# Performance work log

Measured on AMD Instinct MI355X. Metric: run time of the kernel, lower is better.

The kernel has to match this reference:

```python
import jax, jax.numpy as jnp
import numpy as np

EPS = 1e-12  # torch F.normalize eps


def _l1_normalize(x, axis):
    denom = jnp.maximum(jnp.sum(jnp.abs(x), axis=axis, keepdims=True), EPS)
    return x / denom


def setup_inputs() -> dict:
    key = jax.random.key(0)
    k1, k2, k3, k4, k5 = jax.random.split(key, 5)
    B, N, M, F_atom, F_bond, F_out = 16, 1024, 12, 128, 32, 128
    stdv = 1.0 / np.sqrt(F_out)
    atom = jax.random.normal(k1, (B, N, F_atom), dtype=jnp.float32)
    bond = jax.random.normal(k2, (B, N, M, F_bond), dtype=jnp.float32)
    adj_matrix = jax.random.randint(k3, (B, N, M), 0, N, dtype=jnp.int64)
    weight_atom_1 = jax.random.uniform(k4, (F_atom, F_out), dtype=jnp.float32, minval=-stdv, maxval=stdv)
    bias_atom_1 = jax.random.uniform(k5, (F_out,), dtype=jnp.float32, minval=-stdv, maxval=stdv)
    return {
        "atom": atom,
        "bond": bond,
        "adj_matrix": adj_matrix,
        "weight_atom_1": weight_atom_1,
        "bias_atom_1": bias_atom_1,
    }


def reference(atom, bond, adj_matrix, weight_atom_1, bias_atom_1):
    # atom: (B,N,F); bond: (B,N,M,Fb); adj_matrix: (B,N,M)
    # Per-batch neighbor gather: atom_neighbor[b,n,m] = atom[b, adj[b,n,m]]
    atom_neighbor = jax.vmap(lambda a, idx: a[idx])(atom, adj_matrix)  # (B,N,M,F)
    atom_neighbor = jnp.mean(atom_neighbor, axis=-2)  # (B,N,F)

    # Bond-norm chain
    bond_norm = jnp.sqrt(jnp.sum(bond * bond, axis=-1))       # (B,N,M) L2 norm
    bond_norm = bond_norm ** (-2.0)                            # inverse square
    bond_norm = _l1_normalize(bond_norm, axis=-1)              # over M
    bond_norm = jnp.prod(bond_norm, axis=2)                    # (B,N)
    bond_norm = _l1_normalize(bond_norm, axis=0)               # over B
    bond_norm = bond_norm ** (-1.0)
    bond_norm = _l1_normalize(bond_norm, axis=1)               # over N

    atom_update = (atom + atom_neighbor) * bond_norm[:, :, None]
    atom_update = jnp.matmul(atom_update, weight_atom_1) + bias_atom_1
    return jax.nn.relu(atom_update)
```

## Files before the change

kernel.cpp:

```cpp
#include <hip/hip_runtime.h>
#include <hip/hip_bf16.h>

#define EPS 1e-12f

typedef __bf16 bf16x8 __attribute__((ext_vector_type(8)));
typedef float  f32x4  __attribute__((ext_vector_type(4)));


__global__ __launch_bounds__(256) void k_bond(const float* __restrict__ bond,
                                              const float* __restrict__ W,
                                              float* __restrict__ p_out,
                                              __bf16* __restrict__ Wt) {
    const int t = threadIdx.x;
    if (blockIdx.x < 256) {
        const int gtid = blockIdx.x * 256 + t;
        const int row  = gtid >> 2;
        const int q    = gtid & 3;
        const float* base = bond + (size_t)row * 384 + q * 96;

        float x[3];
#pragma unroll
        for (int mm = 0; mm < 3; ++mm) {
            float s = 0.f;
#pragma unroll
            for (int j = 0; j < 8; ++j) {
                f32x4 v = *(const f32x4*)(base + mm * 32 + j * 4);
                s = fmaf(v.x, v.x, s);
                s = fmaf(v.y, v.y, s);
                s = fmaf(v.z, v.z, s);
                s = fmaf(v.w, v.w, s);
            }
            x[mm] = 1.0f / s;
        }
        float sum  = x[0] + x[1] + x[2];
        float prod = x[0] * x[1] * x[2];
        sum  += __shfl_xor(sum, 1);  prod *= __shfl_xor(prod, 1);
        sum  += __shfl_xor(sum, 2);  prod *= __shfl_xor(prod, 2);
        if (q == 0) {
            float d   = fmaxf(sum, EPS);
            float d2  = d * d;
            float d3  = d2 * d;
            float d6  = d3 * d3;
            float d12 = d6 * d6;
            p_out[row] = prod / d12;
        }
    } else {
        const int base = (blockIdx.x - 256) * 4096;
#pragma unroll
        for (int i = 0; i < 16; ++i) {
            int idx = base + t + 256 * i;
            int k = idx >> 7, j = idx & 127;
            Wt[j * 128 + k] = (__bf16)W[idx];
        }
    }
}

__global__ __launch_bounds__(256) void k_main(const float* __restrict__ atom,
                                              const int* __restrict__ adj,
                                              const float* __restrict__ p,
                                              const __bf16* __restrict__ Wt,
                                              const float* __restrict__ bias,
                                              float* __restrict__ out) {
    __shared__ __bf16 uA[32][136];
    __shared__ float  sScale[32];
    __shared__ int    sAdj[32 * 12];
    __shared__ float  red[4];

    const int t = threadIdx.x;
    const int rowbase = blockIdx.x * 32;
    const int b = rowbase >> 10;

    for (int idx = t; idx < 32 * 12; idx += 256) sAdj[idx] = adj[rowbase * 12 + idx];

    float S_part = 0.f;
#pragma unroll
    for (int i = 0; i < 4; ++i) {
        int n = t + 256 * i;
        float cs = 0.f;
#pragma unroll
        for (int bb = 0; bb < 16; ++bb) cs += p[bb * 1024 + n];
        S_part += fmaxf(cs, EPS) / p[b * 1024 + n];
    }
#pragma unroll
    for (int off = 32; off >= 1; off >>= 1) S_part += __shfl_xor(S_part, off);
    if ((t & 63) == 0) red[t >> 6] = S_part;
    __syncthreads();
    const float S = fmaxf(red[0] + red[1] + red[2] + red[3], EPS);
    if (t < 32) {
        int nl = (rowbase & 1023) + t;
        float cs = 0.f;
#pragma unroll
        for (int bb = 0; bb < 16; ++bb) cs += p[bb * 1024 + nl];
        sScale[t] = (fmaxf(cs, EPS) / p[rowbase + t]) / S;
    }
    __syncthreads();

    {
        const int j = t & 127;
        const int half = t >> 7;
        const float* atomB = atom + (size_t)b * (1024 * 128);
#pragma unroll 4
        for (int r = half; r < 32; r += 2) {
            float accn = 0.f;
#pragma unroll
            for (int m = 0; m < 12; ++m) {
                int idx = sAdj[r * 12 + m];
                accn += atomB[idx * 128 + j];
            }
            float u = (atom[(size_t)(rowbase + r) * 128 + j] + accn * (1.0f / 12.0f)) * sScale[r];
            uA[r][j] = (__bf16)u;
        }
    }
    __syncthreads();

    const int wave = t >> 6, lane = t & 63;
    const int r0 = (wave >> 1) * 16;
    const int c0 = (wave & 1) * 64;
    const int quad = lane >> 4, lrow = lane & 15;

    bf16x8 aF[4];
#pragma unroll
    for (int kc = 0; kc < 4; ++kc)
        aF[kc] = *(const bf16x8*)&uA[r0 + lrow][kc * 32 + quad * 8];

    f32x4 acc[4];
#pragma unroll
    for (int nt = 0; nt < 4; ++nt) acc[nt] = (f32x4){0.f, 0.f, 0.f, 0.f};

#pragma unroll
    for (int nt = 0; nt < 4; ++nt) {
        const int col = c0 + nt * 16 + lrow;
        const __bf16* wb = Wt + col * 128 + quad * 8;
#pragma unroll
        for (int kc = 0; kc < 4; ++kc) {
            bf16x8 bF = *(const bf16x8*)(wb + kc * 32);
            acc[nt] = __builtin_amdgcn_mfma_f32_16x16x32_bf16(aF[kc], bF, acc[nt], 0, 0, 0);
        }
    }

#pragma unroll
    for (int nt = 0; nt < 4; ++nt) {
        const int col = c0 + nt * 16 + lrow;
        const float bv = bias[col];
#pragma unroll
        for (int i = 0; i < 4; ++i) {
            const int r = r0 + quad * 4 + i;
            float v = fmaxf(acc[nt][i] + bv, 0.f);
            __builtin_nontemporal_store(v, &out[(size_t)(rowbase + r) * 128 + col]);
        }
    }
}

extern "C" void kernel_launch(void* const* d_in, const int* in_sizes, int n_in,
                              void* d_out, int out_size, void* d_ws, size_t ws_size,
                              hipStream_t stream) {
    const float* atom = (const float*)d_in[0];
    const float* bond = (const float*)d_in[1];
    const int*   adj  = (const int*)d_in[2];
    const float* W    = (const float*)d_in[3];
    const float* bias = (const float*)d_in[4];
    float* out = (float*)d_out;

    char* ws = (char*)d_ws;
    float*  p  = (float*)ws;
    __bf16* Wt = (__bf16*)(ws + 65536);

    hipLaunchKernelGGL(k_bond, dim3(260), dim3(256), 0, stream, bond, W, p, Wt);
    hipLaunchKernelGGL(k_main, dim3(512), dim3(256), 0, stream, atom, adj, p, Wt, bias, out);
}
```

Measured before the change: 104.5 us.

## Vectorize neighbor gather, move row scale after MFMA, overlap p loads

Measured after the change: 116.8 us. 11.8% more time.

```diff
diff --git a/kernel.cpp b/kernel.cpp
--- a/kernel.cpp
+++ b/kernel.cpp
@@ -4,6 +4,7 @@
 #define EPS 1e-12f
 
 typedef __bf16 bf16x8 __attribute__((ext_vector_type(8)));
+typedef __bf16 bf16x4 __attribute__((ext_vector_type(4)));
 typedef float  f32x4  __attribute__((ext_vector_type(4)));
 
 
@@ -24,7 +25,7 @@
             float s = 0.f;
 #pragma unroll
             for (int j = 0; j < 8; ++j) {
-                f32x4 v = *(const f32x4*)(base + mm * 32 + j * 4);
+                f32x4 v = __builtin_nontemporal_load((const f32x4*)(base + mm * 32 + j * 4));
                 s = fmaf(v.x, v.x, s);
                 s = fmaf(v.y, v.y, s);
                 s = fmaf(v.z, v.z, s);
@@ -38,11 +39,8 @@
         sum  += __shfl_xor(sum, 2);  prod *= __shfl_xor(prod, 2);
         if (q == 0) {
             float d   = fmaxf(sum, EPS);
-            float d2  = d * d;
-            float d3  = d2 * d;
-            float d6  = d3 * d3;
-            float d12 = d6 * d6;
-            p_out[row] = prod / d12;
+            float d2  = d * d, d3 = d2 * d, d6 = d3 * d3;
+            p_out[row] = prod / (d6 * d6);
         }
     } else {
         const int base = (blockIdx.x - 256) * 4096;
@@ -62,56 +60,66 @@
                                               const float* __restrict__ bias,
                                               float* __restrict__ out) {
     __shared__ __bf16 uA[32][136];
-    __shared__ float  sScale[32];
+    __shared__ float  sScale[32] __attribute__((aligned(16)));
     __shared__ int    sAdj[32 * 12];
     __shared__ float  red[4];
 
     const int t = threadIdx.x;
     const int rowbase = blockIdx.x * 32;
     const int b = rowbase >> 10;
+    const int nlo = rowbase & 1023;
+
+    const int n0 = t * 4;
+    f32x4 cs = {0.f, 0.f, 0.f, 0.f};
+    f32x4 pv[16];
+#pragma unroll
+    for (int bb = 0; bb < 16; ++bb) pv[bb] = *(const f32x4*)(p + bb * 1024 + n0);
 
     for (int idx = t; idx < 32 * 12; idx += 256) sAdj[idx] = adj[rowbase * 12 + idx];
+    __syncthreads();
 
-    float S_part = 0.f;
+    const int jc = (t & 31) * 4;
+    const int rg = t >> 5;
+    const float* atomB = atom + (size_t)b * (1024 * 128);
+    f32x4 own[4], accn[4];
 #pragma unroll
     for (int i = 0; i < 4; ++i) {
-        int n = t + 256 * i;
-        float cs = 0.f;
+        const int r = rg + i * 8;
+        f32x4 a = {0.f, 0.f, 0.f, 0.f};
 #pragma unroll
-        for (int bb = 0; bb < 16; ++bb) cs += p[bb * 1024 + n];
-        S_part += fmaxf(cs, EPS) / p[b * 1024 + n];
+        for (int m = 0; m < 12; ++m) {
+            int idx = sAdj[r * 12 + m];
+            a += *(const f32x4*)(atomB + (size_t)idx * 128 + jc);
+        }
+        accn[i] = a;
+        own[i]  = *(const f32x4*)(atomB + (size_t)(nlo + r) * 128 + jc);
     }
+
+#pragma unroll
+    for (int bb = 0; bb < 16; ++bb) cs += pv[bb];
+    f32x4 pb = pv[b];
+    f32x4 r4;
+    r4.x = fmaxf(cs.x, EPS) / pb.x;
+    r4.y = fmaxf(cs.y, EPS) / pb.y;
+    r4.z = fmaxf(cs.z, EPS) / pb.z;
+    r4.w = fmaxf(cs.w, EPS) / pb.w;
+    float S_part = r4.x + r4.y + r4.z + r4.w;
 #pragma unroll
     for (int off = 32; off >= 1; off >>= 1) S_part += __shfl_xor(S_part, off);
     if ((t & 63) == 0) red[t >> 6] = S_part;
-    __syncthreads();
-    const float S = fmaxf(red[0] + red[1] + red[2] + red[3], EPS);
-    if (t < 32) {
-        int nl = (rowbase & 1023) + t;
-        float cs = 0.f;
+
 #pragma unroll
-        for (int bb = 0; bb < 16; ++bb) cs += p[bb * 1024 + nl];
-        sScale[t] = (fmaxf(cs, EPS) / p[rowbase + t]) / S;
+    for (int i = 0; i < 4; ++i) {
+        const int r = rg + i * 8;
+        f32x4 u = own[i] + accn[i] * (1.0f / 12.0f);
+        bf16x4 ub;
+        ub.x = (__bf16)u.x; ub.y = (__bf16)u.y; ub.z = (__bf16)u.z; ub.w = (__bf16)u.w;
+        *(bf16x4*)&uA[r][jc] = ub;
     }
     __syncthreads();
 
-    {
-        const int j = t & 127;
-        const int half = t >> 7;
-        const float* atomB = atom + (size_t)b * (1024 * 128);
-#pragma unroll 4
-        for (int r = half; r < 32; r += 2) {
-            float accn = 0.f;
-#pragma unroll
-            for (int m = 0; m < 12; ++m) {
-                int idx = sAdj[r * 12 + m];
-                accn += atomB[idx * 128 + j];
-            }
-            float u = (atom[(size_t)(rowbase + r) * 128 + j] + accn * (1.0f / 12.0f)) * sScale[r];
-            uA[r][j] = (__bf16)u;
-        }
-    }
-    __syncthreads();
+    const float invS = 1.0f / fmaxf(red[0] + red[1] + red[2] + red[3], EPS);
+    if (n0 >= nlo && n0 < nlo + 32) *(f32x4*)&sScale[n0 - nlo] = r4 * invS;
 
     const int wave = t >> 6, lane = t & 63;
     const int r0 = (wave >> 1) * 16;
@@ -137,6 +145,7 @@
             acc[nt] = __builtin_amdgcn_mfma_f32_16x16x32_bf16(aF[kc], bF, acc[nt], 0, 0, 0);
         }
     }
+    __syncthreads();
 
 #pragma unroll
     for (int nt = 0; nt < 4; ++nt) {
@@ -145,7 +154,7 @@
 #pragma unroll
         for (int i = 0; i < 4; ++i) {
             const int r = r0 + quad * 4 + i;
-            float v = fmaxf(acc[nt][i] + bv, 0.f);
+            float v = fmaxf(fmaf(sScale[r], acc[nt][i], bv), 0.f);
             __builtin_nontemporal_store(v, &out[(size_t)(rowbase + r) * 128 + col]);
         }
     }
```
